# Optimization experiments

Hardware: AMD Instinct MI355X
Metric: run time of the kernel (lower is better)

## Reference

```python
import jax, jax.numpy as jnp
import numpy as np

N = 100000
E = 1600000
E_PAIR = 100000
D_IN = 128
D_H = 128


def _sage_mean(x, src, dst, W_neigh, W_self, b):
    # DGL SAGEConv('mean'): out = fc_self(h_dst) + fc_neigh(mean_{u in N(v)} h_u) + bias
    n = x.shape[0]
    msg_sum = jax.ops.segment_sum(x[src], dst, num_segments=n)          # [N, d]
    deg = jax.ops.segment_sum(jnp.ones(src.shape, x.dtype), dst, num_segments=n)
    h_neigh = msg_sum / jnp.maximum(deg, 1.0)[:, None]
    return x @ W_self.T + h_neigh @ W_neigh.T + b


def setup_inputs() -> dict:
    key = jax.random.key(0)
    ks = jax.random.split(key, 16)
    def lin(k, fan_out, fan_in):
        s = 1.0 / np.sqrt(fan_in)
        return jax.random.uniform(k, (fan_out, fan_in), jnp.float32, -s, s)
    inp = {
        'x': jax.random.normal(ks[0], (N, D_IN), jnp.float32),
        'edge_src': jax.random.randint(ks[1], (E,), 0, N),
        'edge_dst': jax.random.randint(ks[2], (E,), 0, N),
        'pos_src': jax.random.randint(ks[3], (E_PAIR,), 0, N),
        'pos_dst': jax.random.randint(ks[4], (E_PAIR,), 0, N),
        'neg_src': jax.random.randint(ks[5], (E_PAIR,), 0, N),
        'neg_dst': jax.random.randint(ks[6], (E_PAIR,), 0, N),
        # SAGEConv layer 1 (in_feats -> n_hidden)
        'W1_neigh': lin(ks[7], D_H, D_IN),
        'W1_self': lin(ks[8], D_H, D_IN),
        'b1': jnp.zeros((D_H,), jnp.float32),
        # SAGEConv layer 2 (n_hidden -> n_hidden)
        'W2_neigh': lin(ks[9], D_H, D_H),
        'W2_self': lin(ks[10], D_H, D_H),
        'b2': jnp.zeros((D_H,), jnp.float32),
        # predictor MLP: Linear(2h->h) ReLU Linear(h->h) ReLU Linear(h->1)
        'P1_w': lin(ks[11], D_H, 2 * D_H),
        'P1_b': jnp.zeros((D_H,), jnp.float32),
        'P2_w': lin(ks[12], D_H, D_H),
        'P2_b': jnp.zeros((D_H,), jnp.float32),
        'P3_w': lin(ks[13], 1, D_H),
        'P3_b': jnp.zeros((1,), jnp.float32),
    }
    return inp


def _predict(h_src, h_dst, P1_w, P1_b, P2_w, P2_b, P3_w, P3_b):
    h = jnp.concatenate([h_src, h_dst], axis=1)
    h = jax.nn.relu(h @ P1_w.T + P1_b)
    h = jax.nn.relu(h @ P2_w.T + P2_b)
    return h @ P3_w.T + P3_b


def reference(x, edge_src, edge_dst, pos_src, pos_dst, neg_src, neg_dst,
              W1_neigh, W1_self, b1, W2_neigh, W2_self, b2,
              P1_w, P1_b, P2_w, P2_b, P3_w, P3_b):
    h = _sage_mean(x, edge_src, edge_dst, W1_neigh, W1_self, b1)
    h = jax.nn.relu(h)
    h = _sage_mean(h, edge_src, edge_dst, W2_neigh, W2_self, b2)
    h_pos = _predict(h[pos_src], h[pos_dst], P1_w, P1_b, P2_w, P2_b, P3_w, P3_b)
    h_neg = _predict(h[neg_src], h[neg_dst], P1_w, P1_b, P2_w, P2_b, P3_w, P3_b)
    return (h_pos, h_neg)
```

## Files before the change

kernel.cpp:

```cpp
#include <hip/hip_runtime.h>
#include <hip/hip_bf16.h>
#include <hip/hip_fp16.h>


#define D 128
#define NR 512
#define PART_CHUNK 4096
#define LDA 40
#define LDH2 136

typedef _Float16 f16x8 __attribute__((ext_vector_type(8)));
typedef float f32x4 __attribute__((ext_vector_type(4)));

__global__ __launch_bounds__(256) void k_regcount(
    const int* __restrict__ dst, int* __restrict__ region_cnt, int e, int bound) {
    __shared__ int s[NR];
    for (int i = threadIdx.x; i < NR; i += 256) s[i] = 0;
    __syncthreads();
    for (int i = blockIdx.x * 256 + threadIdx.x; i < e; i += gridDim.x * 256)
        atomicAdd(&s[dst[i] / bound], 1);
    __syncthreads();
    for (int i = threadIdx.x; i < NR; i += 256)
        if (s[i]) atomicAdd(&region_cnt[i], s[i]);
}

__global__ void k_regbase(const int* __restrict__ region_cnt,
                          int* __restrict__ region_base, int* __restrict__ region_cursor) {
    if (threadIdx.x == 0 && blockIdx.x == 0) {
        int run = 0;
        for (int r = 0; r < NR; ++r) {
            region_base[r] = run; region_cursor[r] = run; run += region_cnt[r];
        }
        region_base[NR] = run;
    }
}

__global__ __launch_bounds__(256) void k_regpart(
    const int* __restrict__ src, const int* __restrict__ dst,
    unsigned int* __restrict__ eout, int* __restrict__ region_cursor, int e, int bound) {
    __shared__ int s_cnt[NR];
    __shared__ int s_base[NR];
    for (int c0 = blockIdx.x * PART_CHUNK; c0 < e; c0 += gridDim.x * PART_CHUNK) {
        int cend = min(c0 + PART_CHUNK, e);
        for (int i = threadIdx.x; i < NR; i += 256) s_cnt[i] = 0;
        __syncthreads();
        for (int i = c0 + threadIdx.x; i < cend; i += 256)
            atomicAdd(&s_cnt[dst[i] / bound], 1);
        __syncthreads();
        for (int i = threadIdx.x; i < NR; i += 256)
            s_base[i] = s_cnt[i] ? atomicAdd(&region_cursor[i], s_cnt[i]) : 0;
        __syncthreads();
        for (int i = threadIdx.x; i < NR; i += 256) s_cnt[i] = 0;
        __syncthreads();
        for (int i = c0 + threadIdx.x; i < cend; i += 256) {
            int d = dst[i];
            int r = d / bound;
            unsigned int doff = (unsigned int)(d - r * bound);
            int p = atomicAdd(&s_cnt[r], 1);
            eout[s_base[r] + p] = (unsigned int)src[i] | (doff << 20);
        }
        __syncthreads();
    }
}

__global__ __launch_bounds__(256) void k_rowoff(
    const unsigned int* __restrict__ ep, const int* __restrict__ region_base,
    int* __restrict__ row_off, int n, int bound) {
    int r = blockIdx.x;
    int rlo = r * bound;
    if (threadIdx.x == 0 && r == 0) row_off[n] = region_base[NR];
    if (rlo >= n) return;
    int nn = min(bound, n - rlo);
    __shared__ int s_deg[256];
    __shared__ int s_scan[256];
    if (threadIdx.x < 256) s_deg[threadIdx.x] = 0;
    __syncthreads();
    int beg = region_base[r], end = region_base[r + 1];
    for (int i = beg + threadIdx.x; i < end; i += 256)
        atomicAdd(&s_deg[ep[i] >> 20], 1);
    __syncthreads();
    int v = (threadIdx.x < nn) ? s_deg[threadIdx.x] : 0;
    s_scan[threadIdx.x] = v;
    __syncthreads();
    #pragma unroll
    for (int off = 1; off < 256; off <<= 1) {
        int add = (threadIdx.x >= off) ? s_scan[threadIdx.x - off] : 0;
        __syncthreads();
        s_scan[threadIdx.x] += add;
        __syncthreads();
    }
    if (threadIdx.x < nn)
        row_off[rlo + threadIdx.x] = region_base[r] +
            (threadIdx.x ? s_scan[threadIdx.x - 1] : 0);
}

__global__ __launch_bounds__(256) void k_scatter3(
    const unsigned int* __restrict__ ep, const int* __restrict__ region_base,
    const int* __restrict__ row_off, int* __restrict__ csr, int n, int bound) {
    int r = blockIdx.x;
    int rlo = r * bound;
    if (rlo >= n) return;
    int nn = min(bound, n - rlo);
    __shared__ int s_cur[256];
    __shared__ int s_ro[256];
    if (threadIdx.x < nn) {
        s_cur[threadIdx.x] = 0;
        s_ro[threadIdx.x] = row_off[rlo + threadIdx.x];
    }
    __syncthreads();
    int beg = region_base[r], end = region_base[r + 1];
    for (int i = beg + threadIdx.x; i < end; i += 256) {
        unsigned int v = ep[i];
        int doff = v >> 20;
        int srcn = v & 0xFFFFF;
        int p = atomicAdd(&s_cur[doff], 1);
        csr[s_ro[doff] + p] = srcn;
    }
}

__global__ void k_cvt_f16(const float* __restrict__ src, _Float16* __restrict__ dst, int n8) {
    int i = blockIdx.x * 256 + threadIdx.x;
    if (i >= n8) return;
    const float4* s4 = (const float4*)src;
    float4 a = s4[2 * i], b = s4[2 * i + 1];
    f16x8 h;
    h[0] = (_Float16)a.x; h[1] = (_Float16)a.y; h[2] = (_Float16)a.z; h[3] = (_Float16)a.w;
    h[4] = (_Float16)b.x; h[5] = (_Float16)b.y; h[6] = (_Float16)b.z; h[7] = (_Float16)b.w;
    *(f16x8*)(dst + 8 * i) = h;
}

__global__ void k_cvt_weights(
    const float* __restrict__ W1s, const float* __restrict__ W1n,
    const float* __restrict__ W2s, const float* __restrict__ W2n,
    const float* __restrict__ P1w, const float* __restrict__ P2w,
    _Float16* __restrict__ Ws1f, _Float16* __restrict__ Wn1f,
    _Float16* __restrict__ Ws2f, _Float16* __restrict__ Wn2f,
    _Float16* __restrict__ P1cf, _Float16* __restrict__ P2wf) {
    int g = blockIdx.x * 256 + threadIdx.x;
    if (g >= 14336) return;
    const float* src; _Float16* dst; int off;
    if (g >= 8192 && g < 12288) {
        int u = g - 8192;
        int o = u >> 4, col = (u & 15) * 8;
        src = P1w + (size_t)(o & 127) * 256 + ((o >> 7) * 128) + col;
        float4 a = *(const float4*)src, b = *(const float4*)(src + 4);
        f16x8 h;
        h[0] = (_Float16)a.x; h[1] = (_Float16)a.y; h[2] = (_Float16)a.z; h[3] = (_Float16)a.w;
        h[4] = (_Float16)b.x; h[5] = (_Float16)b.y; h[6] = (_Float16)b.z; h[7] = (_Float16)b.w;
        *(f16x8*)(P1cf + (size_t)u * 8) = h;
        return;
    }
    if      (g <  2048) { src = W1s; dst = Ws1f; off = g; }
    else if (g <  4096) { src = W1n; dst = Wn1f; off = g - 2048; }
    else if (g <  6144) { src = W2s; dst = Ws2f; off = g - 4096; }
    else if (g <  8192) { src = W2n; dst = Wn2f; off = g - 6144; }
    else                { src = P2w; dst = P2wf; off = g - 12288; }
    const float4* s4 = (const float4*)src;
    float4 a = s4[2 * off], b = s4[2 * off + 1];
    f16x8 h;
    h[0] = (_Float16)a.x; h[1] = (_Float16)a.y; h[2] = (_Float16)a.z; h[3] = (_Float16)a.w;
    h[4] = (_Float16)b.x; h[5] = (_Float16)b.y; h[6] = (_Float16)b.z; h[7] = (_Float16)b.w;
    *(f16x8*)(dst + 8 * off) = h;
}

__global__ __launch_bounds__(256) void k_agg(
    const _Float16* __restrict__ Xf, const int* __restrict__ row_off,
    const int* __restrict__ csr, _Float16* __restrict__ Aggf, int n_nodes) {
    int g = blockIdx.x * 16 + (threadIdx.x >> 4);
    if (g >= n_nodes) return;
    int l = threadIdx.x & 15;
    int beg = row_off[g], end = row_off[g + 1];
    float acc[8] = {0.f, 0.f, 0.f, 0.f, 0.f, 0.f, 0.f, 0.f};
    int i = beg;
    for (; i + 4 <= end; i += 4) {
        int s0 = csr[i], s1 = csr[i + 1], s2 = csr[i + 2], s3 = csr[i + 3];
        f16x8 v0 = *(const f16x8*)(Xf + (size_t)s0 * D + l * 8);
        f16x8 v1 = *(const f16x8*)(Xf + (size_t)s1 * D + l * 8);
        f16x8 v2 = *(const f16x8*)(Xf + (size_t)s2 * D + l * 8);
        f16x8 v3 = *(const f16x8*)(Xf + (size_t)s3 * D + l * 8);
        #pragma unroll
        for (int j = 0; j < 8; ++j)
            acc[j] += ((float)v0[j] + (float)v1[j]) + ((float)v2[j] + (float)v3[j]);
    }
    for (; i < end; ++i) {
        int s0 = csr[i];
        f16x8 v0 = *(const f16x8*)(Xf + (size_t)s0 * D + l * 8);
        #pragma unroll
        for (int j = 0; j < 8; ++j) acc[j] += (float)v0[j];
    }
    float inv = 1.0f / fmaxf((float)(end - beg), 1.0f);
    f16x8 o;
    #pragma unroll
    for (int j = 0; j < 8; ++j) o[j] = (_Float16)(acc[j] * inv);
    *(f16x8*)(Aggf + (size_t)g * D + l * 8) = o;
}

__global__ __launch_bounds__(512) void k_transform(
    const _Float16* __restrict__ Xf, const _Float16* __restrict__ Aggf,
    const _Float16* __restrict__ Wsf, const _Float16* __restrict__ Wnf,
    const float* __restrict__ bias, _Float16* __restrict__ outf,
    int n_rows, int do_relu) {
    __shared__ _Float16 s_a[2][128 * LDA];
    __shared__ _Float16 s_b[2][128 * LDA];
    int tid = threadIdx.x;
    int w = tid >> 6, l = tid & 63;
    int wr = w >> 1, wc = w & 1;
    int l15 = l & 15, lk = l >> 4;
    int n0 = blockIdx.x * 128;
    int r = tid >> 2, q = tid & 3;
    int rstage = n0 + r; if (rstage >= n_rows) rstage = n_rows - 1;

    f32x4 acc[2][4];
    #pragma unroll
    for (int i = 0; i < 2; ++i)
        #pragma unroll
        for (int j = 0; j < 4; ++j) acc[i][j] = (f32x4){0.f, 0.f, 0.f, 0.f};

    int a_off = (wr * 32 + l15) * LDA + lk * 8;
    int b_off = (wc * 64 + l15) * LDA + lk * 8;
    int st_off = r * LDA + q * 8;

    {
        f16x8 av = *(const f16x8*)(Xf + (size_t)rstage * D + q * 8);
        f16x8 wv = *(const f16x8*)(Wsf + (size_t)r * D + q * 8);
        *(f16x8*)(&s_a[0][st_off]) = av;
        *(f16x8*)(&s_b[0][st_off]) = wv;
    }
    __syncthreads();

    for (int c = 0; c < 8; ++c) {
        int b = c & 1;
        f16x8 av, wv;
        if (c < 7) {
            int cn = c + 1;
            const _Float16* asrc = (cn < 4) ? Xf : Aggf;
            const _Float16* wsrc = (cn < 4) ? Wsf : Wnf;
            int kb = (cn & 3) * 32;
            av = *(const f16x8*)(asrc + (size_t)rstage * D + kb + q * 8);
            wv = *(const f16x8*)(wsrc + (size_t)r * D + kb + q * 8);
        }
        f16x8 af[2], bf[4];
        af[0] = *(const f16x8*)(&s_a[b][a_off]);
        af[1] = *(const f16x8*)(&s_a[b][a_off + 16 * LDA]);
        #pragma unroll
        for (int j = 0; j < 4; ++j) bf[j] = *(const f16x8*)(&s_b[b][b_off + j * 16 * LDA]);
        #pragma unroll
        for (int i = 0; i < 2; ++i)
            #pragma unroll
            for (int j = 0; j < 4; ++j)
                acc[i][j] = __builtin_amdgcn_mfma_f32_16x16x32_f16(af[i], bf[j], acc[i][j], 0, 0, 0);
        if (c < 7) {
            *(f16x8*)(&s_a[b ^ 1][st_off]) = av;
            *(f16x8*)(&s_b[b ^ 1][st_off]) = wv;
        }
        __syncthreads();
    }

    #pragma unroll
    for (int j = 0; j < 4; ++j) {
        int col = wc * 64 + j * 16 + l15;
        float bv = bias[col];
        #pragma unroll
        for (int i = 0; i < 2; ++i) {
            int rowb = n0 + wr * 32 + i * 16 + lk * 4;
            #pragma unroll
            for (int v = 0; v < 4; ++v) {
                int row = rowb + v;
                if (row < n_rows) {
                    float xv = acc[i][j][v] + bv;
                    if (do_relu) xv = fmaxf(xv, 0.f);
                    outf[(size_t)row * D + col] = (_Float16)xv;
                }
            }
        }
    }
}

__global__ __launch_bounds__(512) void k_pre(
    const _Float16* __restrict__ Hf, const _Float16* __restrict__ P1cf,
    _Float16* __restrict__ Pre, int n_rows) {
    __shared__ _Float16 s_a[64 * LDA];
    __shared__ _Float16 s_b[256 * LDA];
    int tid = threadIdx.x;
    int w = tid >> 6, l = tid & 63;
    int wr = w >> 2, wc = w & 3;
    int l15 = l & 15, lk = l >> 4;
    int n0 = blockIdx.x * 64;

    f32x4 acc[2][4];
    #pragma unroll
    for (int i = 0; i < 2; ++i)
        #pragma unroll
        for (int j = 0; j < 4; ++j) acc[i][j] = (f32x4){0.f, 0.f, 0.f, 0.f};

    int a_off = (wr * 32 + l15) * LDA + lk * 8;

    for (int c = 0; c < 4; ++c) {
        int kb = c * 32;
        __syncthreads();
        if (tid < 256) {
            int r = tid >> 2, q = tid & 3;
            int rstage = n0 + r; if (rstage >= n_rows) rstage = n_rows - 1;
            *(f16x8*)(&s_a[r * LDA + q * 8]) =
                *(const f16x8*)(Hf + (size_t)rstage * D + kb + q * 8);
        }
        #pragma unroll
        for (int e = 0; e < 2; ++e) {
            int idx = tid + e * 512;
            int o = idx >> 2, q = idx & 3;
            *(f16x8*)(&s_b[o * LDA + q * 8]) =
                *(const f16x8*)(P1cf + (size_t)o * 128 + kb + q * 8);
        }
        __syncthreads();
        f16x8 af[2], bf[4];
        af[0] = *(const f16x8*)(&s_a[a_off]);
        af[1] = *(const f16x8*)(&s_a[a_off + 16 * LDA]);
        #pragma unroll
        for (int j = 0; j < 4; ++j)
            bf[j] = *(const f16x8*)(&s_b[(wc * 64 + j * 16 + l15) * LDA + lk * 8]);
        #pragma unroll
        for (int i = 0; i < 2; ++i)
            #pragma unroll
            for (int j = 0; j < 4; ++j)
                acc[i][j] = __builtin_amdgcn_mfma_f32_16x16x32_f16(af[i], bf[j], acc[i][j], 0, 0, 0);
    }

    #pragma unroll
    for (int j = 0; j < 4; ++j) {
        int col = wc * 64 + j * 16 + l15;
        #pragma unroll
        for (int i = 0; i < 2; ++i) {
            int rowb = n0 + wr * 32 + i * 16 + lk * 4;
            #pragma unroll
            for (int v = 0; v < 4; ++v) {
                int row = rowb + v;
                if (row < n_rows)
                    Pre[(size_t)row * 256 + col] = (_Float16)acc[i][j][v];
            }
        }
    }
}

__global__ __launch_bounds__(256) void k_mlp(
    const _Float16* __restrict__ Pre,
    const int* __restrict__ pos_src, const int* __restrict__ pos_dst,
    const int* __restrict__ neg_src, const int* __restrict__ neg_dst,
    const float* __restrict__ P1b,
    const _Float16* __restrict__ P2wf, const float* __restrict__ P2b,
    const float* __restrict__ P3w, const float* __restrict__ P3b,
    float* __restrict__ out, int EP) {
    __shared__ _Float16 s_h1[64 * LDH2];
    __shared__ _Float16 s_b[2][128 * LDA];
    __shared__ float s_red[64 * 2];
    __shared__ int s_node[128];
    int tid = threadIdx.x;
    int w = tid >> 6, l = tid & 63;
    int wr = w >> 1, wc = w & 1;
    int l15 = l & 15, lk = l >> 4;
    int p0 = blockIdx.x * 64;
    int twoEP = 2 * EP;

    if (tid < 128) {
        int p = p0 + (tid & 63);
        if (p >= twoEP) p = twoEP - 1;
        int node;
        if (tid < 64) node = (p < EP) ? pos_src[p] : neg_src[p - EP];
        else          node = (p < EP) ? pos_dst[p] : neg_dst[p - EP];
        s_node[tid] = node;
    }
    __syncthreads();

    #pragma unroll
    for (int e = 0; e < 4; ++e) {
        int idx = tid + e * 256;
        int pr = idx >> 4, u = idx & 15;
        int sn = s_node[pr], dn = s_node[64 + pr];
        f16x8 a = *(const f16x8*)(Pre + (size_t)sn * 256 + u * 8);
        f16x8 b = *(const f16x8*)(Pre + (size_t)dn * 256 + 128 + u * 8);
        float4 b0 = *(const float4*)(P1b + u * 8);
        float4 b1 = *(const float4*)(P1b + u * 8 + 4);
        float bb[8] = {b0.x, b0.y, b0.z, b0.w, b1.x, b1.y, b1.z, b1.w};
        f16x8 h;
        #pragma unroll
        for (int j = 0; j < 8; ++j)
            h[j] = (_Float16)fmaxf((float)a[j] + (float)b[j] + bb[j], 0.f);
        *(f16x8*)(&s_h1[pr * LDH2 + u * 8]) = h;
    }
    #pragma unroll
    for (int e = 0; e < 2; ++e) {
        int idx = tid + e * 256;
        int o = idx >> 2, q = idx & 3;
        *(f16x8*)(&s_b[0][o * LDA + q * 8]) = *(const f16x8*)(P2wf + (size_t)o * D + q * 8);
    }
    __syncthreads();

    f32x4 acc2[2][4];
    #pragma unroll
    for (int i = 0; i < 2; ++i)
        #pragma unroll
        for (int j = 0; j < 4; ++j) acc2[i][j] = (f32x4){0.f, 0.f, 0.f, 0.f};

    for (int c = 0; c < 4; ++c) {
        int b = c & 1;
        f16x8 nw[2];
        if (c < 3) {
            #pragma unroll
            for (int e = 0; e < 2; ++e) {
                int idx = tid + e * 256;
                int o = idx >> 2, q = idx & 3;
                nw[e] = *(const f16x8*)(P2wf + (size_t)o * D + (c + 1) * 32 + q * 8);
            }
        }
        f16x8 af[2], bf[4];
        af[0] = *(const f16x8*)(&s_h1[(wr * 32 + l15) * LDH2 + c * 32 + lk * 8]);
        af[1] = *(const f16x8*)(&s_h1[(wr * 32 + 16 + l15) * LDH2 + c * 32 + lk * 8]);
        #pragma unroll
        for (int j = 0; j < 4; ++j)
            bf[j] = *(const f16x8*)(&s_b[b][(wc * 64 + j * 16 + l15) * LDA + lk * 8]);
        #pragma unroll
        for (int i = 0; i < 2; ++i)
            #pragma unroll
            for (int j = 0; j < 4; ++j)
                acc2[i][j] = __builtin_amdgcn_mfma_f32_16x16x32_f16(af[i], bf[j], acc2[i][j], 0, 0, 0);
        if (c < 3) {
            #pragma unroll
            for (int e = 0; e < 2; ++e) {
                int idx = tid + e * 256;
                int o = idx >> 2, q = idx & 3;
                *(f16x8*)(&s_b[b ^ 1][o * LDA + q * 8]) = nw[e];
            }
        }
        __syncthreads();
    }

    float b2v[4], pw[4];
    #pragma unroll
    for (int j = 0; j < 4; ++j) {
        int col = wc * 64 + j * 16 + l15;
        b2v[j] = P2b[col];
        pw[j] = P3w[col];
    }
    #pragma unroll
    for (int i = 0; i < 2; ++i) {
        #pragma unroll
        for (int v = 0; v < 4; ++v) {
            float s = 0.f;
            #pragma unroll
            for (int j = 0; j < 4; ++j)
                s += fmaxf(acc2[i][j][v] + b2v[j], 0.f) * pw[j];
            s += __shfl_xor(s, 1);
            s += __shfl_xor(s, 2);
            s += __shfl_xor(s, 4);
            s += __shfl_xor(s, 8);
            if (l15 == 0)
                s_red[(wr * 32 + i * 16 + lk * 4 + v) * 2 + wc] = s;
        }
    }
    __syncthreads();
    if (tid < 64) {
        int p = p0 + tid;
        if (p < twoEP) out[p] = s_red[tid * 2] + s_red[tid * 2 + 1] + P3b[0];
    }
}

static inline size_t align_up(size_t x, size_t a) { return (x + a - 1) & ~(a - 1); }

extern "C" void kernel_launch(void* const* d_in, const int* in_sizes, int n_in,
                              void* d_out, int out_size, void* d_ws, size_t ws_size,
                              hipStream_t stream) {
    const float* x        = (const float*)d_in[0];
    const int*   edge_src = (const int*)d_in[1];
    const int*   edge_dst = (const int*)d_in[2];
    const int*   pos_src  = (const int*)d_in[3];
    const int*   pos_dst  = (const int*)d_in[4];
    const int*   neg_src  = (const int*)d_in[5];
    const int*   neg_dst  = (const int*)d_in[6];
    const float* W1n = (const float*)d_in[7];
    const float* W1s = (const float*)d_in[8];
    const float* b1  = (const float*)d_in[9];
    const float* W2n = (const float*)d_in[10];
    const float* W2s = (const float*)d_in[11];
    const float* b2  = (const float*)d_in[12];
    const float* P1w = (const float*)d_in[13];
    const float* P1b = (const float*)d_in[14];
    const float* P2w = (const float*)d_in[15];
    const float* P2b = (const float*)d_in[16];
    const float* P3w = (const float*)d_in[17];
    const float* P3b = (const float*)d_in[18];
    float* out = (float*)d_out;

    const int N = in_sizes[0] / D;
    const int E = in_sizes[1];
    const int EP = in_sizes[3];
    const int bound = (N + NR - 1) / NR;

    char* ws = (char*)d_ws;
    size_t off = 0;
    int* row_off = (int*)(ws + off); off = align_up(off + (size_t)(N + 1) * 4, 256);
    int* regmeta = (int*)(ws + off); off = align_up(off + (size_t)(3 * NR + 8) * 4, 256);
    int* csr     = (int*)(ws + off); off = align_up(off + (size_t)E * 4, 256);
    unsigned int* epart = (unsigned int*)(ws + off); off = align_up(off + (size_t)E * 4, 256);
    _Float16* xf   = (_Float16*)(ws + off); off = align_up(off + (size_t)N * D * 2, 256);
    _Float16* aggf = (_Float16*)(ws + off); off = align_up(off + (size_t)N * D * 2, 256);
    _Float16* h1f  = (_Float16*)(ws + off); off = align_up(off + (size_t)N * D * 2, 256);
    _Float16* h2f  = (_Float16*)(ws + off); off = align_up(off + (size_t)N * D * 2, 256);
    _Float16* Ws1f = (_Float16*)(ws + off); off = align_up(off + (size_t)D * D * 2, 256);
    _Float16* Wn1f = (_Float16*)(ws + off); off = align_up(off + (size_t)D * D * 2, 256);
    _Float16* Ws2f = (_Float16*)(ws + off); off = align_up(off + (size_t)D * D * 2, 256);
    _Float16* Wn2f = (_Float16*)(ws + off); off = align_up(off + (size_t)D * D * 2, 256);
    _Float16* P1cf = (_Float16*)(ws + off); off = align_up(off + (size_t)2 * D * D * 2, 256);
    _Float16* P2wf = (_Float16*)(ws + off); off = align_up(off + (size_t)D * D * 2, 256);
    (void)ws_size;

    _Float16* Pre = xf;

    int* region_cnt    = regmeta;
    int* region_base   = regmeta + NR;
    int* region_cursor = regmeta + 2 * NR + 4;

    hipMemsetAsync(region_cnt, 0, NR * 4, stream);
    k_regcount<<<128, 256, 0, stream>>>(edge_dst, region_cnt, E, bound);
    k_regbase<<<1, 1, 0, stream>>>(region_cnt, region_base, region_cursor);
    k_regpart<<<(E + PART_CHUNK - 1) / PART_CHUNK, 256, 0, stream>>>(
        edge_src, edge_dst, epart, region_cursor, E, bound);
    k_rowoff<<<NR, 256, 0, stream>>>(epart, region_base, row_off, N, bound);
    k_scatter3<<<NR, 256, 0, stream>>>(epart, region_base, row_off, csr, N, bound);

    k_cvt_f16<<<(N * D / 8 + 255) / 256, 256, 0, stream>>>(x, xf, N * D / 8);
    k_cvt_weights<<<56, 256, 0, stream>>>(W1s, W1n, W2s, W2n, P1w, P2w,
                                          Ws1f, Wn1f, Ws2f, Wn2f, P1cf, P2wf);

    const int ngrid = (N + 127) / 128;
    const int pgrid = (2 * EP + 63) / 64;

    k_agg<<<(N + 15) / 16, 256, 0, stream>>>(xf, row_off, csr, aggf, N);
    k_transform<<<ngrid, 512, 0, stream>>>(xf, aggf, Ws1f, Wn1f, b1, h1f, N, 1);
    k_agg<<<(N + 15) / 16, 256, 0, stream>>>(h1f, row_off, csr, aggf, N);
    k_transform<<<ngrid, 512, 0, stream>>>(h1f, aggf, Ws2f, Wn2f, b2, h2f, N, 0);

    k_pre<<<(N + 63) / 64, 512, 0, stream>>>(h2f, P1cf, Pre, N);
    k_mlp<<<pgrid, 256, 0, stream>>>(Pre, pos_src, pos_dst, neg_src, neg_dst,
                                     P1b, P2wf, P2b, P3w, P3b, out, EP);
}
```

Baseline: 317.2 us.

## Fuse neighbor aggregation into SAGE transform kernel via shared-memory staging

Merges the separate mean-aggregation kernel and the MFMA transform kernel into one kernel. Each block first gathers and averages neighbor features for its 128 rows into an LDS tile, then runs the GEMM reading the aggregated operand directly from LDS. This removes the round-trip write and read of the N×128 aggregate buffer and one launch per layer. In exchange, LDS use per block grows and the gather phase now runs inside a 512-thread block sized for the GEMM, which can lower occupancy and the latency hiding available to the irregular gathers.

```diff
diff --git a/kernel.cpp b/kernel.cpp
--- a/kernel.cpp
+++ b/kernel.cpp
@@ -7,6 +7,7 @@
 #define NR 512
 #define PART_CHUNK 4096
 #define LDA 40
+#define LDAGG 136
 #define LDH2 136
 
 typedef _Float16 f16x8 __attribute__((ext_vector_type(8)));
@@ -163,50 +164,57 @@
     *(f16x8*)(dst + 8 * off) = h;
 }
 
-__global__ __launch_bounds__(256) void k_agg(
+__global__ __launch_bounds__(512) void k_sage(
     const _Float16* __restrict__ Xf, const int* __restrict__ row_off,
-    const int* __restrict__ csr, _Float16* __restrict__ Aggf, int n_nodes) {
-    int g = blockIdx.x * 16 + (threadIdx.x >> 4);
-    if (g >= n_nodes) return;
-    int l = threadIdx.x & 15;
-    int beg = row_off[g], end = row_off[g + 1];
-    float acc[8] = {0.f, 0.f, 0.f, 0.f, 0.f, 0.f, 0.f, 0.f};
-    int i = beg;
-    for (; i + 4 <= end; i += 4) {
-        int s0 = csr[i], s1 = csr[i + 1], s2 = csr[i + 2], s3 = csr[i + 3];
-        f16x8 v0 = *(const f16x8*)(Xf + (size_t)s0 * D + l * 8);
-        f16x8 v1 = *(const f16x8*)(Xf + (size_t)s1 * D + l * 8);
-        f16x8 v2 = *(const f16x8*)(Xf + (size_t)s2 * D + l * 8);
-        f16x8 v3 = *(const f16x8*)(Xf + (size_t)s3 * D + l * 8);
-        #pragma unroll
-        for (int j = 0; j < 8; ++j)
-            acc[j] += ((float)v0[j] + (float)v1[j]) + ((float)v2[j] + (float)v3[j]);
-    }
-    for (; i < end; ++i) {
-        int s0 = csr[i];
-        f16x8 v0 = *(const f16x8*)(Xf + (size_t)s0 * D + l * 8);
-        #pragma unroll
-        for (int j = 0; j < 8; ++j) acc[j] += (float)v0[j];
-    }
-    float inv = 1.0f / fmaxf((float)(end - beg), 1.0f);
-    f16x8 o;
-    #pragma unroll
-    for (int j = 0; j < 8; ++j) o[j] = (_Float16)(acc[j] * inv);
-    *(f16x8*)(Aggf + (size_t)g * D + l * 8) = o;
-}
-
-__global__ __launch_bounds__(512) void k_transform(
-    const _Float16* __restrict__ Xf, const _Float16* __restrict__ Aggf,
+    const int* __restrict__ csr,
     const _Float16* __restrict__ Wsf, const _Float16* __restrict__ Wnf,
     const float* __restrict__ bias, _Float16* __restrict__ outf,
     int n_rows, int do_relu) {
+    __shared__ _Float16 s_agg[128 * LDAGG];
     __shared__ _Float16 s_a[2][128 * LDA];
     __shared__ _Float16 s_b[2][128 * LDA];
     int tid = threadIdx.x;
+    int n0 = blockIdx.x * 128;
+
+    {
+        int grp = tid >> 4, l = tid & 15;
+        #pragma unroll
+        for (int it = 0; it < 4; ++it) {
+            int r = grp + it * 32;
+            int g = n0 + r;
+            float acc[8] = {0.f, 0.f, 0.f, 0.f, 0.f, 0.f, 0.f, 0.f};
+            float inv = 0.f;
+            if (g < n_rows) {
+                int beg = row_off[g], end = row_off[g + 1];
+                int i = beg;
+                for (; i + 4 <= end; i += 4) {
+                    int s0 = csr[i], s1 = csr[i + 1], s2 = csr[i + 2], s3 = csr[i + 3];
+                    f16x8 v0 = *(const f16x8*)(Xf + (size_t)s0 * D + l * 8);
+                    f16x8 v1 = *(const f16x8*)(Xf + (size_t)s1 * D + l * 8);
+                    f16x8 v2 = *(const f16x8*)(Xf + (size_t)s2 * D + l * 8);
+                    f16x8 v3 = *(const f16x8*)(Xf + (size_t)s3 * D + l * 8);
+                    #pragma unroll
+                    for (int j = 0; j < 8; ++j)
+                        acc[j] += ((float)v0[j] + (float)v1[j]) + ((float)v2[j] + (float)v3[j]);
+                }
+                for (; i < end; ++i) {
+                    int s0 = csr[i];
+                    f16x8 v0 = *(const f16x8*)(Xf + (size_t)s0 * D + l * 8);
+                    #pragma unroll
+                    for (int j = 0; j < 8; ++j) acc[j] += (float)v0[j];
+                }
+                inv = 1.0f / fmaxf((float)(end - beg), 1.0f);
+            }
+            f16x8 o;
+            #pragma unroll
+            for (int j = 0; j < 8; ++j) o[j] = (_Float16)(acc[j] * inv);
+            *(f16x8*)(s_agg + r * LDAGG + l * 8) = o;
+        }
+    }
+
     int w = tid >> 6, l = tid & 63;
     int wr = w >> 1, wc = w & 1;
     int l15 = l & 15, lk = l >> 4;
-    int n0 = blockIdx.x * 128;
     int r = tid >> 2, q = tid & 3;
     int rstage = n0 + r; if (rstage >= n_rows) rstage = n_rows - 1;
 
@@ -217,31 +225,37 @@
         for (int j = 0; j < 4; ++j) acc[i][j] = (f32x4){0.f, 0.f, 0.f, 0.f};
 
     int a_off = (wr * 32 + l15) * LDA + lk * 8;
+    int agg_off = (wr * 32 + l15) * LDAGG + lk * 8;
     int b_off = (wc * 64 + l15) * LDA + lk * 8;
     int st_off = r * LDA + q * 8;
 
-    {
-        f16x8 av = *(const f16x8*)(Xf + (size_t)rstage * D + q * 8);
-        f16x8 wv = *(const f16x8*)(Wsf + (size_t)r * D + q * 8);
-        *(f16x8*)(&s_a[0][st_off]) = av;
-        *(f16x8*)(&s_b[0][st_off]) = wv;
-    }
+    f16x8 av0 = *(const f16x8*)(Xf + (size_t)rstage * D + q * 8);
+    f16x8 wv0 = *(const f16x8*)(Wsf + (size_t)r * D + q * 8);
+    *(f16x8*)(&s_a[0][st_off]) = av0;
+    *(f16x8*)(&s_b[0][st_off]) = wv0;
     __syncthreads();
 
     for (int c = 0; c < 8; ++c) {
         int b = c & 1;
         f16x8 av, wv;
+        bool pf_a = (c < 3);
         if (c < 7) {
             int cn = c + 1;
-            const _Float16* asrc = (cn < 4) ? Xf : Aggf;
             const _Float16* wsrc = (cn < 4) ? Wsf : Wnf;
             int kb = (cn & 3) * 32;
-            av = *(const f16x8*)(asrc + (size_t)rstage * D + kb + q * 8);
+            if (pf_a)
+                av = *(const f16x8*)(Xf + (size_t)rstage * D + kb + q * 8);
             wv = *(const f16x8*)(wsrc + (size_t)r * D + kb + q * 8);
         }
         f16x8 af[2], bf[4];
-        af[0] = *(const f16x8*)(&s_a[b][a_off]);
-        af[1] = *(const f16x8*)(&s_a[b][a_off + 16 * LDA]);
+        if (c < 4) {
+            af[0] = *(const f16x8*)(&s_a[b][a_off]);
+            af[1] = *(const f16x8*)(&s_a[b][a_off + 16 * LDA]);
+        } else {
+            int kb = (c - 4) * 32;
+            af[0] = *(const f16x8*)(s_agg + agg_off + kb);
+            af[1] = *(const f16x8*)(s_agg + agg_off + 16 * LDAGG + kb);
+        }
         #pragma unroll
         for (int j = 0; j < 4; ++j) bf[j] = *(const f16x8*)(&s_b[b][b_off + j * 16 * LDA]);
         #pragma unroll
@@ -250,7 +264,7 @@
             for (int j = 0; j < 4; ++j)
                 acc[i][j] = __builtin_amdgcn_mfma_f32_16x16x32_f16(af[i], bf[j], acc[i][j], 0, 0, 0);
         if (c < 7) {
-            *(f16x8*)(&s_a[b ^ 1][st_off]) = av;
+            if (pf_a) *(f16x8*)(&s_a[b ^ 1][st_off]) = av;
             *(f16x8*)(&s_b[b ^ 1][st_off]) = wv;
         }
         __syncthreads();
@@ -511,6 +525,7 @@
     _Float16* P1cf = (_Float16*)(ws + off); off = align_up(off + (size_t)2 * D * D * 2, 256);
     _Float16* P2wf = (_Float16*)(ws + off); off = align_up(off + (size_t)D * D * 2, 256);
     (void)ws_size;
+    (void)aggf;
 
     _Float16* Pre = xf;
 
@@ -533,10 +548,8 @@
     const int ngrid = (N + 127) / 128;
     const int pgrid = (2 * EP + 63) / 64;
 
-    k_agg<<<(N + 15) / 16, 256, 0, stream>>>(xf, row_off, csr, aggf, N);
-    k_transform<<<ngrid, 512, 0, stream>>>(xf, aggf, Ws1f, Wn1f, b1, h1f, N, 1);
-    k_agg<<<(N + 15) / 16, 256, 0, stream>>>(h1f, row_off, csr, aggf, N);
-    k_transform<<<ngrid, 512, 0, stream>>>(h1f, aggf, Ws2f, Wn2f, b2, h2f, N, 0);
+    k_sage<<<ngrid, 512, 0, stream>>>(xf, row_off, csr, Ws1f, Wn1f, b1, h1f, N, 1);
+    k_sage<<<ngrid, 512, 0, stream>>>(h1f, row_off, csr, Ws2f, Wn2f, b2, h2f, N, 0);
 
     k_pre<<<(N + 63) / 64, 512, 0, stream>>>(h2f, P1cf, Pre, N);
     k_mlp<<<pgrid, 256, 0, stream>>>(Pre, pos_src, pos_dst, neg_src, neg_dst,
```

After: 322.1 us. Within noise of the previous version (+1.5%).

## Fuse setup conversions with region count, merge rowoff/scatter, unroll aggregation by 8

Applied to the files above, without the earlier changes.

Merges the x/weight fp16 conversion kernels and the dst region histogram into one launch, using block-index ranges to dispatch roles. Fuses the row-offset scan and CSR scatter into one kernel that caches each region's edges in shared memory, avoiding a second global read of the partitioned edges. Deepens the aggregation gather unroll to 8 neighbors for more memory-level parallelism. These add shared memory and register pressure, and fall back to global reads when a region has more edges than the shared buffer holds.

```diff
diff --git a/kernel.cpp b/kernel.cpp
--- a/kernel.cpp
+++ b/kernel.cpp
@@ -12,12 +12,59 @@
 typedef _Float16 f16x8 __attribute__((ext_vector_type(8)));
 typedef float f32x4 __attribute__((ext_vector_type(4)));
 
-__global__ __launch_bounds__(256) void k_regcount(
+__device__ __forceinline__ void cvt8(const float* src, _Float16* dst, int off8) {
+    const float4* s4 = (const float4*)src;
+    float4 a = s4[2 * off8], b = s4[2 * off8 + 1];
+    f16x8 h;
+    h[0] = (_Float16)a.x; h[1] = (_Float16)a.y; h[2] = (_Float16)a.z; h[3] = (_Float16)a.w;
+    h[4] = (_Float16)b.x; h[5] = (_Float16)b.y; h[6] = (_Float16)b.z; h[7] = (_Float16)b.w;
+    *(f16x8*)(dst + 8 * off8) = h;
+}
+
+__global__ __launch_bounds__(256) void k_setup(
+    const float* __restrict__ x, _Float16* __restrict__ xf, int n8, int nb_x,
+    const float* __restrict__ W1s, const float* __restrict__ W1n,
+    const float* __restrict__ W2s, const float* __restrict__ W2n,
+    const float* __restrict__ P1w, const float* __restrict__ P2w,
+    _Float16* __restrict__ Ws1f, _Float16* __restrict__ Wn1f,
+    _Float16* __restrict__ Ws2f, _Float16* __restrict__ Wn2f,
+    _Float16* __restrict__ P1cf, _Float16* __restrict__ P2wf,
     const int* __restrict__ dst, int* __restrict__ region_cnt, int e, int bound) {
+    int b = blockIdx.x;
+    if (b < nb_x) {
+        int i = b * 256 + threadIdx.x;
+        if (i < n8) cvt8(x, xf, i);
+        return;
+    }
+    b -= nb_x;
+    if (b < 56) {
+        int g = b * 256 + threadIdx.x;
+        if (g >= 14336) return;
+        if (g >= 8192 && g < 12288) {
+            int u = g - 8192;
+            int o = u >> 4, col = (u & 15) * 8;
+            const float* src = P1w + (size_t)(o & 127) * 256 + ((o >> 7) * 128) + col;
+            float4 a = *(const float4*)src, bb = *(const float4*)(src + 4);
+            f16x8 h;
+            h[0] = (_Float16)a.x; h[1] = (_Float16)a.y; h[2] = (_Float16)a.z; h[3] = (_Float16)a.w;
+            h[4] = (_Float16)bb.x; h[5] = (_Float16)bb.y; h[6] = (_Float16)bb.z; h[7] = (_Float16)bb.w;
+            *(f16x8*)(P1cf + (size_t)u * 8) = h;
+            return;
+        }
+        const float* src; _Float16* dstp; int off;
+        if      (g <  2048) { src = W1s; dstp = Ws1f; off = g; }
+        else if (g <  4096) { src = W1n; dstp = Wn1f; off = g - 2048; }
+        else if (g <  6144) { src = W2s; dstp = Ws2f; off = g - 4096; }
+        else if (g <  8192) { src = W2n; dstp = Wn2f; off = g - 6144; }
+        else                { src = P2w; dstp = P2wf; off = g - 12288; }
+        cvt8(src, dstp, off);
+        return;
+    }
+    b -= 56;
     __shared__ int s[NR];
     for (int i = threadIdx.x; i < NR; i += 256) s[i] = 0;
     __syncthreads();
-    for (int i = blockIdx.x * 256 + threadIdx.x; i < e; i += gridDim.x * 256)
+    for (int i = b * 256 + threadIdx.x; i < e; i += 128 * 256)
         atomicAdd(&s[dst[i] / bound], 1);
     __syncthreads();
     for (int i = threadIdx.x; i < NR; i += 256)
@@ -63,21 +110,28 @@
     }
 }
 
-__global__ __launch_bounds__(256) void k_rowoff(
+#define EMAX 4608
+__global__ __launch_bounds__(256) void k_rowoff_scatter(
     const unsigned int* __restrict__ ep, const int* __restrict__ region_base,
-    int* __restrict__ row_off, int n, int bound) {
+    int* __restrict__ row_off, int* __restrict__ csr, int n, int bound) {
     int r = blockIdx.x;
     int rlo = r * bound;
     if (threadIdx.x == 0 && r == 0) row_off[n] = region_base[NR];
     if (rlo >= n) return;
     int nn = min(bound, n - rlo);
+    __shared__ unsigned int s_e[EMAX];
     __shared__ int s_deg[256];
     __shared__ int s_scan[256];
-    if (threadIdx.x < 256) s_deg[threadIdx.x] = 0;
-    __syncthreads();
+    __shared__ int s_cur[256];
     int beg = region_base[r], end = region_base[r + 1];
-    for (int i = beg + threadIdx.x; i < end; i += 256)
-        atomicAdd(&s_deg[ep[i] >> 20], 1);
+    int cnt = end - beg;
+    bool fit = (cnt <= EMAX);
+    if (fit)
+        for (int i = threadIdx.x; i < cnt; i += 256) s_e[i] = ep[beg + i];
+    s_deg[threadIdx.x] = 0;
+    __syncthreads();
+    for (int i = threadIdx.x; i < cnt; i += 256)
+        atomicAdd(&s_deg[(fit ? s_e[i] : ep[beg + i]) >> 20], 1);
     __syncthreads();
     int v = (threadIdx.x < nn) ? s_deg[threadIdx.x] : 0;
     s_scan[threadIdx.x] = v;
@@ -89,78 +143,16 @@
         s_scan[threadIdx.x] += add;
         __syncthreads();
     }
-    if (threadIdx.x < nn)
-        row_off[rlo + threadIdx.x] = region_base[r] +
-            (threadIdx.x ? s_scan[threadIdx.x - 1] : 0);
-}
-
-__global__ __launch_bounds__(256) void k_scatter3(
-    const unsigned int* __restrict__ ep, const int* __restrict__ region_base,
-    const int* __restrict__ row_off, int* __restrict__ csr, int n, int bound) {
-    int r = blockIdx.x;
-    int rlo = r * bound;
-    if (rlo >= n) return;
-    int nn = min(bound, n - rlo);
-    __shared__ int s_cur[256];
-    __shared__ int s_ro[256];
-    if (threadIdx.x < nn) {
-        s_cur[threadIdx.x] = 0;
-        s_ro[threadIdx.x] = row_off[rlo + threadIdx.x];
-    }
-    __syncthreads();
-    int beg = region_base[r], end = region_base[r + 1];
-    for (int i = beg + threadIdx.x; i < end; i += 256) {
-        unsigned int v = ep[i];
-        int doff = v >> 20;
-        int srcn = v & 0xFFFFF;
+    int base = beg + (threadIdx.x ? s_scan[threadIdx.x - 1] : 0);
+    s_cur[threadIdx.x] = base;
+    if (threadIdx.x < nn) row_off[rlo + threadIdx.x] = base;
+    __syncthreads();
+    for (int i = threadIdx.x; i < cnt; i += 256) {
+        unsigned int e2 = fit ? s_e[i] : ep[beg + i];
+        int doff = e2 >> 20;
         int p = atomicAdd(&s_cur[doff], 1);
-        csr[s_ro[doff] + p] = srcn;
-    }
-}
-
-__global__ void k_cvt_f16(const float* __restrict__ src, _Float16* __restrict__ dst, int n8) {
-    int i = blockIdx.x * 256 + threadIdx.x;
-    if (i >= n8) return;
-    const float4* s4 = (const float4*)src;
-    float4 a = s4[2 * i], b = s4[2 * i + 1];
-    f16x8 h;
-    h[0] = (_Float16)a.x; h[1] = (_Float16)a.y; h[2] = (_Float16)a.z; h[3] = (_Float16)a.w;
-    h[4] = (_Float16)b.x; h[5] = (_Float16)b.y; h[6] = (_Float16)b.z; h[7] = (_Float16)b.w;
-    *(f16x8*)(dst + 8 * i) = h;
-}
-
-__global__ void k_cvt_weights(
-    const float* __restrict__ W1s, const float* __restrict__ W1n,
-    const float* __restrict__ W2s, const float* __restrict__ W2n,
-    const float* __restrict__ P1w, const float* __restrict__ P2w,
-    _Float16* __restrict__ Ws1f, _Float16* __restrict__ Wn1f,
-    _Float16* __restrict__ Ws2f, _Float16* __restrict__ Wn2f,
-    _Float16* __restrict__ P1cf, _Float16* __restrict__ P2wf) {
-    int g = blockIdx.x * 256 + threadIdx.x;
-    if (g >= 14336) return;
-    const float* src; _Float16* dst; int off;
-    if (g >= 8192 && g < 12288) {
-        int u = g - 8192;
-        int o = u >> 4, col = (u & 15) * 8;
-        src = P1w + (size_t)(o & 127) * 256 + ((o >> 7) * 128) + col;
-        float4 a = *(const float4*)src, b = *(const float4*)(src + 4);
-        f16x8 h;
-        h[0] = (_Float16)a.x; h[1] = (_Float16)a.y; h[2] = (_Float16)a.z; h[3] = (_Float16)a.w;
-        h[4] = (_Float16)b.x; h[5] = (_Float16)b.y; h[6] = (_Float16)b.z; h[7] = (_Float16)b.w;
-        *(f16x8*)(P1cf + (size_t)u * 8) = h;
-        return;
-    }
-    if      (g <  2048) { src = W1s; dst = Ws1f; off = g; }
-    else if (g <  4096) { src = W1n; dst = Wn1f; off = g - 2048; }
-    else if (g <  6144) { src = W2s; dst = Ws2f; off = g - 4096; }
-    else if (g <  8192) { src = W2n; dst = Wn2f; off = g - 6144; }
-    else                { src = P2w; dst = P2wf; off = g - 12288; }
-    const float4* s4 = (const float4*)src;
-    float4 a = s4[2 * off], b = s4[2 * off + 1];
-    f16x8 h;
-    h[0] = (_Float16)a.x; h[1] = (_Float16)a.y; h[2] = (_Float16)a.z; h[3] = (_Float16)a.w;
-    h[4] = (_Float16)b.x; h[5] = (_Float16)b.y; h[6] = (_Float16)b.z; h[7] = (_Float16)b.w;
-    *(f16x8*)(dst + 8 * off) = h;
+        csr[p] = e2 & 0xFFFFF;
+    }
 }
 
 __global__ __launch_bounds__(256) void k_agg(
@@ -172,26 +164,36 @@
     int beg = row_off[g], end = row_off[g + 1];
     float acc[8] = {0.f, 0.f, 0.f, 0.f, 0.f, 0.f, 0.f, 0.f};
     int i = beg;
-    for (; i + 4 <= end; i += 4) {
-        int s0 = csr[i], s1 = csr[i + 1], s2 = csr[i + 2], s3 = csr[i + 3];
+    for (; i + 8 <= end; i += 8) {
+        int si[8];
+        #pragma unroll
+        for (int j = 0; j < 8; ++j) si[j] = csr[i + j];
+        f16x8 vv[8];
+        #pragma unroll
+        for (int j = 0; j < 8; ++j)
+            vv[j] = *(const f16x8*)(Xf + (size_t)si[j] * D + l * 8);
+        #pragma unroll
+        for (int j = 0; j < 8; ++j)
+            #pragma unroll
+            for (int k = 0; k < 8; ++k) acc[k] += (float)vv[j][k];
+    }
+    for (; i + 2 <= end; i += 2) {
+        int s0 = csr[i], s1 = csr[i + 1];
         f16x8 v0 = *(const f16x8*)(Xf + (size_t)s0 * D + l * 8);
         f16x8 v1 = *(const f16x8*)(Xf + (size_t)s1 * D + l * 8);
-        f16x8 v2 = *(const f16x8*)(Xf + (size_t)s2 * D + l * 8);
-        f16x8 v3 = *(const f16x8*)(Xf + (size_t)s3 * D + l * 8);
-        #pragma unroll
-        for (int j = 0; j < 8; ++j)
-            acc[j] += ((float)v0[j] + (float)v1[j]) + ((float)v2[j] + (float)v3[j]);
-    }
-    for (; i < end; ++i) {
+        #pragma unroll
+        for (int k = 0; k < 8; ++k) acc[k] += (float)v0[k] + (float)v1[k];
+    }
+    if (i < end) {
         int s0 = csr[i];
         f16x8 v0 = *(const f16x8*)(Xf + (size_t)s0 * D + l * 8);
         #pragma unroll
-        for (int j = 0; j < 8; ++j) acc[j] += (float)v0[j];
+        for (int k = 0; k < 8; ++k) acc[k] += (float)v0[k];
     }
     float inv = 1.0f / fmaxf((float)(end - beg), 1.0f);
     f16x8 o;
     #pragma unroll
-    for (int j = 0; j < 8; ++j) o[j] = (_Float16)(acc[j] * inv);
+    for (int k = 0; k < 8; ++k) o[k] = (_Float16)(acc[k] * inv);
     *(f16x8*)(Aggf + (size_t)g * D + l * 8) = o;
 }
 
@@ -518,17 +520,18 @@
     int* region_base   = regmeta + NR;
     int* region_cursor = regmeta + 2 * NR + 4;
 
+    const int n8 = N * D / 8;
+    const int nb_x = (n8 + 255) / 256;
+
     hipMemsetAsync(region_cnt, 0, NR * 4, stream);
-    k_regcount<<<128, 256, 0, stream>>>(edge_dst, region_cnt, E, bound);
+    k_setup<<<nb_x + 56 + 128, 256, 0, stream>>>(
+        x, xf, n8, nb_x, W1s, W1n, W2s, W2n, P1w, P2w,
+        Ws1f, Wn1f, Ws2f, Wn2f, P1cf, P2wf,
+        edge_dst, region_cnt, E, bound);
     k_regbase<<<1, 1, 0, stream>>>(region_cnt, region_base, region_cursor);
     k_regpart<<<(E + PART_CHUNK - 1) / PART_CHUNK, 256, 0, stream>>>(
         edge_src, edge_dst, epart, region_cursor, E, bound);
-    k_rowoff<<<NR, 256, 0, stream>>>(epart, region_base, row_off, N, bound);
-    k_scatter3<<<NR, 256, 0, stream>>>(epart, region_base, row_off, csr, N, bound);
-
-    k_cvt_f16<<<(N * D / 8 + 255) / 256, 256, 0, stream>>>(x, xf, N * D / 8);
-    k_cvt_weights<<<56, 256, 0, stream>>>(W1s, W1n, W2s, W2n, P1w, P2w,
-                                          Ws1f, Wn1f, Ws2f, Wn2f, P1cf, P2wf);
+    k_rowoff_scatter<<<NR, 256, 0, stream>>>(epart, region_base, row_off, csr, N, bound);
 
     const int ngrid = (N + 127) / 128;
     const int pgrid = (2 * EP + 63) / 64;
```

Result: faster. 310.3 us (-2.2%).
